# Optimization experiments

Measured on AMD Instinct MI355X. Metric: run time of the kernel, lower is better.

The kernel has to match this reference:

```python
import jax, jax.numpy as jnp
import numpy as np

SH_C0 = 0.28209479177387814  # DC spherical-harmonic basis constant


def setup_inputs() -> dict:
    key = jax.random.key(0)
    ks = jax.random.split(key, 6)
    b, v, g = 1, 2, 2048
    means = jax.random.normal(ks[0], (b, g, 3), dtype=jnp.float32) * 2.0
    # PSD 3x3 covariances via L @ L^T
    L = jax.random.normal(ks[1], (b, g, 3, 3), dtype=jnp.float32) * 0.2
    covariances = jnp.einsum('bgij,bgkj->bgik', L, L) + 1e-4 * jnp.eye(3, dtype=jnp.float32)
    harmonics = jax.random.normal(ks[2], (b, g, 3, 1), dtype=jnp.float32) * 0.5
    opacities = jax.nn.sigmoid(jax.random.normal(ks[3], (b, g), dtype=jnp.float32))
    # camera-to-world extrinsics: identity rotation, cameras pulled back on -z
    ext = jnp.tile(jnp.eye(4, dtype=jnp.float32), (b, v, 1, 1))
    trans = jnp.array([[0.0, 0.0, -8.0], [0.5, 0.0, -8.0]], dtype=jnp.float32)
    ext = ext.at[:, :, :3, 3].set(trans[None])
    intr = jnp.tile(jnp.array([[1.0, 0.0, 0.5], [0.0, 1.0, 0.5], [0.0, 0.0, 1.0]],
                              dtype=jnp.float32), (b, v, 1, 1))  # normalized intrinsics
    return {"means": means, "covariances": covariances, "harmonics": harmonics,
            "opacities": opacities, "extrinsics": ext, "intrinsics": intr,
            "height": 96, "width": 96}


def _render_one(viewmat, K, means, covs, sh, opac, bg, H, W, near, far):
    # viewmat: world->camera [4,4]; K: pixel intrinsics [3,3]
    R, t = viewmat[:3, :3], viewmat[:3, 3]
    cam = means @ R.T + t                                   # [G,3]
    x, y, z = cam[:, 0], cam[:, 1], cam[:, 2]
    zc = jnp.maximum(z, 1e-6)
    fx, fy, cx, cy = K[0, 0], K[1, 1], K[0, 2], K[1, 2]
    u = fx * x / zc + cx                                    # pixel-space 2D means
    vv = fy * y / zc + cy
    # 3D covariance in camera frame, then EWA projection to 2D
    covc = jnp.einsum('ij,gjk,lk->gil', R, covs, R)         # [G,3,3]
    zero = jnp.zeros_like(z)
    J = jnp.stack([jnp.stack([fx / zc, zero, -fx * x / zc**2], -1),
                   jnp.stack([zero, fy / zc, -fy * y / zc**2], -1)], -2)  # [G,2,3]
    cov2 = jnp.einsum('gij,gjk,glk->gil', J, covc, J)       # [G,2,2]
    a = cov2[:, 0, 0] + 0.3                                 # low-pass dilation
    c = cov2[:, 1, 1] + 0.3
    bq = cov2[:, 0, 1]
    det = a * c - bq * bq
    inv_det = 1.0 / jnp.maximum(det, 1e-12)
    # pixel grid (pixel centers)
    px = jnp.arange(W, dtype=jnp.float32) + 0.5
    py = jnp.arange(H, dtype=jnp.float32) + 0.5
    PX, PY = jnp.meshgrid(px, py)                           # [H,W]
    dx = PX.reshape(-1)[None, :] - u[:, None]               # [G,HW]
    dy = PY.reshape(-1)[None, :] - vv[:, None]
    power = -0.5 * inv_det[:, None] * (c[:, None] * dx * dx + a[:, None] * dy * dy
                                       - 2.0 * bq[:, None] * dx * dy)
    alpha = jnp.clip(opac[:, None] * jnp.exp(jnp.minimum(power, 0.0)), 0.0, 0.999)
    valid = (z > near) & (z < far) & (det > 0.0)
    alpha = alpha * valid[:, None].astype(alpha.dtype)      # [G,HW]
    col = SH_C0 * sh[:, :, 0] + 0.5                         # DC SH -> rgb [G,3]
    # front-to-back alpha compositing in depth order
    order = jnp.argsort(z)
    alpha_s = alpha[order]
    col_s = col[order]
    z_s = z[order]
    cum = jnp.cumprod(1.0 - alpha_s, axis=0)                # [G,HW]
    T = jnp.concatenate([jnp.ones((1, alpha_s.shape[1]), alpha_s.dtype), cum[:-1]], 0)
    w = T * alpha_s                                         # per-gaussian pixel weights
    color = jnp.einsum('gp,gc->cp', w, col_s) + cum[-1][None, :] * bg[:, None]
    depth = jnp.sum(w * z_s[:, None], axis=0)
    return color.reshape(3, H, W), depth.reshape(H, W)


def reference(means, covariances, harmonics, opacities, extrinsics, intrinsics, height, width):
    near0, far0 = 0.1, 100.0
    sf = 1.0 / near0                                        # scale_factor = 10
    bg = jnp.zeros(3, dtype=jnp.float32)                    # background_color
    b, v = extrinsics.shape[:2]
    means_s = means * sf
    covs_s = covariances * (sf * sf)
    ext = extrinsics.at[..., :3, 3].multiply(sf)
    near, far = 1.0, far0 * sf
    ext = ext.reshape(b * v, 4, 4)
    K = intrinsics.reshape(b * v, 3, 3)
    K = K.at[:, 0, :].multiply(float(width)).at[:, 1, :].multiply(float(height))
    viewmats = jnp.linalg.inv(ext)                          # world->camera
    # repeat gaussians over views: 'b g ... -> (b v) g ...'
    m_r = jnp.repeat(means_s, v, axis=0)
    c_r = jnp.repeat(covs_s, v, axis=0)
    s_r = jnp.repeat(harmonics, v, axis=0)
    o_r = jnp.repeat(opacities, v, axis=0)
    render = jax.vmap(lambda vm, Kc, m, cc, s, o:
                      _render_one(vm, Kc, m, cc, s, o, bg, height, width, near, far))
    color, depth = render(viewmats, K, m_r, c_r, s_r, o_r)
    color = jnp.clip(color.reshape(b, v, 3, height, width), 0.0, 1.0)
    depth = depth.reshape(b, v, height, width)
    return color, depth
```

## Files before the change

kernel.cpp:

```cpp
#include <hip/hip_runtime.h>

#define SH_C0 0.28209479177387814f
#define LOG2E 1.4426950408889634f

__device__ __forceinline__ void view_from_ext(const float* e, float R[9], float t[3]) {
  const float sf = 10.0f;
  float a00=e[0],a01=e[1],a02=e[2], a10=e[4],a11=e[5],a12=e[6], a20=e[8],a21=e[9],a22=e[10];
  float tx=e[3]*sf, ty=e[7]*sf, tz=e[11]*sf;
  float c00 =  a11*a22 - a12*a21;
  float c01 = -(a10*a22 - a12*a20);
  float c02 =  a10*a21 - a11*a20;
  float det = a00*c00 + a01*c01 + a02*c02;
  float id = 1.0f/det;
  R[0]=c00*id;               R[1]=(a02*a21-a01*a22)*id; R[2]=(a01*a12-a02*a11)*id;
  R[3]=c01*id;               R[4]=(a00*a22-a02*a20)*id; R[5]=(a02*a10-a00*a12)*id;
  R[6]=c02*id;               R[7]=(a01*a20-a00*a21)*id; R[8]=(a00*a11-a01*a10)*id;
  t[0]=-(R[0]*tx+R[1]*ty+R[2]*tz);
  t[1]=-(R[3]*tx+R[4]*ty+R[5]*tz);
  t[2]=-(R[6]*tx+R[7]*ty+R[8]*tz);
}

__global__ __launch_bounds__(256) void rank_prep_kernel(
    const float* __restrict__ means, const float* __restrict__ covs,
    const float* __restrict__ sh, const float* __restrict__ opac,
    const float* __restrict__ ext, const float* __restrict__ intr,
    float* __restrict__ sorted, int G, float Wf, float Hf) {
  __shared__ float kl[2048];
  __shared__ int ps[4][64];
  int v = blockIdx.y;
  int tid = threadIdx.x;
  float R[9], t3[3];
  view_from_ext(ext + v*16, R, t3);
  for (int i = tid; i < G; i += 256) {
    const float* m = means + (size_t)i*3;
    kl[i] = R[6]*(m[0]*10.0f) + R[7]*(m[1]*10.0f) + R[8]*(m[2]*10.0f) + t3[2];
  }
  __syncthreads();
  int s = tid >> 6, gl = tid & 63;
  int g = blockIdx.x*64 + gl;
  float myz = kl[g];
  int seg = G >> 2;
  int j0 = s * seg;
  int cnt = 0;
  #pragma unroll 16
  for (int j = j0; j < j0 + seg; ++j) {
    float kj = kl[j];
    cnt += (kj < myz || (kj == myz && j < g)) ? 1 : 0;
  }
  ps[s][gl] = cnt;
  __syncthreads();
  if (s != 0) return;
  int rank = ps[0][gl] + ps[1][gl] + ps[2][gl] + ps[3][gl];

  const float* Kv = intr + v*9;
  float fx = Kv[0]*Wf, cx = Kv[2]*Wf;
  float fy = Kv[4]*Hf, cy = Kv[5]*Hf;
  const float* m = means + (size_t)g*3;
  float mx = m[0]*10.0f, my = m[1]*10.0f, mz = m[2]*10.0f;
  float x = R[0]*mx + R[1]*my + R[2]*mz + t3[0];
  float y = R[3]*mx + R[4]*my + R[5]*mz + t3[1];
  float z = R[6]*mx + R[7]*my + R[8]*mz + t3[2];
  float zc = fmaxf(z, 1e-6f);
  float u  = fx*x/zc + cx;
  float vv = fy*y/zc + cy;
  const float* C9 = covs + (size_t)g*9;
  float cs[9];
  #pragma unroll
  for (int q = 0; q < 9; ++q) cs[q] = C9[q]*100.0f;
  float tm[9], M[9];
  #pragma unroll
  for (int r2 = 0; r2 < 3; ++r2)
    #pragma unroll
    for (int c2 = 0; c2 < 3; ++c2)
      tm[r2*3+c2] = R[r2*3+0]*cs[c2] + R[r2*3+1]*cs[3+c2] + R[r2*3+2]*cs[6+c2];
  #pragma unroll
  for (int r2 = 0; r2 < 3; ++r2)
    #pragma unroll
    for (int c2 = 0; c2 < 3; ++c2)
      M[r2*3+c2] = tm[r2*3+0]*R[c2*3+0] + tm[r2*3+1]*R[c2*3+1] + tm[r2*3+2]*R[c2*3+2];
  float j0f = fx/zc, j2f = -fx*x/(zc*zc);
  float j1f = fy/zc, j3f = -fy*y/(zc*zc);
  float c00 = j0f*(M[0]*j0f + M[2]*j2f) + j2f*(M[6]*j0f + M[8]*j2f);
  float c01 = j0f*(M[1]*j1f + M[2]*j3f) + j2f*(M[7]*j1f + M[8]*j3f);
  float c11 = j1f*(M[4]*j1f + M[5]*j3f) + j3f*(M[7]*j1f + M[8]*j3f);
  float a = c00 + 0.3f, c = c11 + 0.3f, bq = c01;
  float det2 = a*c - bq*bq;
  float invd = 1.0f/fmaxf(det2, 1e-12f);
  bool valid = (z > 1.0f) && (z < 1000.0f) && (det2 > 0.0f);
  float op = valid ? opac[g] : 0.0f;
  float* o = sorted + ((size_t)v*G + rank)*12;
  o[0] = u; o[1] = vv;
  o[2] = -0.5f*invd*c*LOG2E;
  o[3] =  invd*bq*LOG2E;
  o[4] = -0.5f*invd*a*LOG2E;
  o[5] = op;
  o[6] = SH_C0*sh[(size_t)g*3+0]+0.5f;
  o[7] = SH_C0*sh[(size_t)g*3+1]+0.5f;
  o[8] = SH_C0*sh[(size_t)g*3+2]+0.5f;
  o[9] = z; o[10] = 0.0f; o[11] = 0.0f;
}

__global__ __launch_bounds__(256) void render_kernel(
    const float4* __restrict__ srt, float4* __restrict__ p4,
    float* __restrict__ pD, int G, int chunkSize, int P, int W) {
  __shared__ float4 sp[128*3];
  int tid = threadIdx.x;
  int view = blockIdx.z, chunk = blockIdx.y;
  int pixBase = blockIdx.x * 1024;
  float pxk[4], pyk[4];
  #pragma unroll
  for (int k = 0; k < 4; ++k) {
    int p = pixBase + tid + k*256;
    pxk[k] = (float)(p % W) + 0.5f;
    pyk[k] = (float)(p / W) + 0.5f;
  }
  float T[4]  = {1.0f,1.0f,1.0f,1.0f};
  float cr[4] = {0,0,0,0}, cg[4] = {0,0,0,0}, cb[4] = {0,0,0,0}, dp[4] = {0,0,0,0};
  int cstart = chunk * chunkSize, cend = cstart + chunkSize;
  for (int g0 = cstart; g0 < cend; g0 += 128) {
    int nt = min(128, cend - g0);
    __syncthreads();
    for (int q = tid; q < nt*3; q += 256)
      sp[q] = srt[((size_t)view*G + g0)*3 + q];
    __syncthreads();
    #pragma unroll 2
    for (int i = 0; i < nt; ++i) {
      float4 q0 = sp[i*3+0], q1 = sp[i*3+1], q2 = sp[i*3+2];
      float u = q0.x, vv = q0.y, A = q0.z, B = q0.w;
      float Cc = q1.x, op = q1.y, r = q1.z, gcol = q1.w;
      float bcol = q2.x, z = q2.y;
      #pragma unroll
      for (int k = 0; k < 4; ++k) {
        float dx = pxk[k] - u, dy = pyk[k] - vv;
        float t1 = fmaf(B, dy, A*dx);
        float pw = fmaf(dx, t1, Cc*dy*dy);
        pw = fminf(pw, 0.0f);
        float al = fminf(op*exp2f(pw), 0.999f);
        float w = T[k]*al;
        cr[k] = fmaf(w, r,    cr[k]);
        cg[k] = fmaf(w, gcol, cg[k]);
        cb[k] = fmaf(w, bcol, cb[k]);
        dp[k] = fmaf(w, z,    dp[k]);
        T[k] *= (1.0f - al);
      }
    }
  }
  size_t base = ((size_t)(view*gridDim.y + chunk))*(size_t)P;
  #pragma unroll
  for (int k = 0; k < 4; ++k) {
    int pix = pixBase + tid + k*256;
    p4[base + pix] = make_float4(T[k], cr[k], cg[k], cb[k]);
    pD[base + pix] = dp[k];
  }
}

template<int NC>
__global__ __launch_bounds__(256) void combine_kernel(
    const float4* __restrict__ p4, const float* __restrict__ pD,
    float* __restrict__ out, int P, int V) {
  int id = blockIdx.x*256 + threadIdx.x;
  if (id >= V*P) return;
  int view = id / P, pix = id - view*P;
  float T = 1.0f, cr = 0, cg = 0, cb = 0, dp = 0;
  #pragma unroll
  for (int c2 = 0; c2 < NC; ++c2) {
    size_t base = ((size_t)(view*NC + c2))*(size_t)P + pix;
    float4 b = p4[base];
    float d  = pD[base];
    cr = fmaf(T, b.y, cr);
    cg = fmaf(T, b.z, cg);
    cb = fmaf(T, b.w, cb);
    dp = fmaf(T, d,   dp);
    T *= b.x;
  }
  out[(size_t)(view*3+0)*P + pix] = fminf(fmaxf(cr, 0.0f), 1.0f);
  out[(size_t)(view*3+1)*P + pix] = fminf(fmaxf(cg, 0.0f), 1.0f);
  out[(size_t)(view*3+2)*P + pix] = fminf(fmaxf(cb, 0.0f), 1.0f);
  out[(size_t)V*3*P + (size_t)view*P + pix] = dp;
}

extern "C" void kernel_launch(void* const* d_in, const int* in_sizes, int n_in,
                              void* d_out, int out_size, void* d_ws, size_t ws_size,
                              hipStream_t stream) {
  const float* means = (const float*)d_in[0];
  const float* covs  = (const float*)d_in[1];
  const float* sh    = (const float*)d_in[2];
  const float* opac  = (const float*)d_in[3];
  const float* ext   = (const float*)d_in[4];
  const float* intr  = (const float*)d_in[5];
  const int G = in_sizes[0] / 3;
  const int V = in_sizes[4] / 16;
  const int H = 96, W = 96, P = H*W;

  char* ws = (char*)d_ws;
  float* sorted = (float*)ws;
  size_t off1 = (((size_t)V*G*12*sizeof(float)) + 255) & ~(size_t)255;
  int NC = 32;
  size_t p4_bytes = (size_t)V*NC*(size_t)P*sizeof(float4);
  float4* p4 = (float4*)(ws + off1);
  size_t off2 = (off1 + p4_bytes + 255) & ~(size_t)255;
  float* pD = (float*)(ws + off2);

  dim3 gr(G/64, V);
  rank_prep_kernel<<<gr, 256, 0, stream>>>(means, covs, sh, opac, ext, intr,
                                           sorted, G, (float)W, (float)H);
  dim3 gc(P/1024, NC, V);
  render_kernel<<<gc, 256, 0, stream>>>((const float4*)sorted, p4, pD, G, G/NC, P, W);
  int cbn = (V*P + 255)/256;
  combine_kernel<32><<<cbn, 256, 0, stream>>>(p4, pD, (float*)d_out, P, V);
}
```

Before: 118.5 us.

## Cull gaussians per 32x32 tile with conservative bound; vectorize rank counting

The render kernel now maps each block to a 32x32 pixel tile and a 64-gaussian chunk. It computes a conservative upper bound on the exponent over the tile and compacts only the surviving gaussians into a shared index list, so the blend loop skips gaussians that cannot contribute. The rank kernel reads depth keys as float4 to cut shared-memory load instructions. The cull threshold of -30 in log2 space drops contributions below roughly 1e-9, a small approximation, and the clamp of the exponent to non-positive values is removed.

Measured after the change: 106.4 us. -10.2%, faster.

```diff
diff --git a/kernel.cpp b/kernel.cpp
--- a/kernel.cpp
+++ b/kernel.cpp
@@ -25,8 +25,9 @@
     const float* __restrict__ sh, const float* __restrict__ opac,
     const float* __restrict__ ext, const float* __restrict__ intr,
     float* __restrict__ sorted, int G, float Wf, float Hf) {
-  __shared__ float kl[2048];
+  __shared__ float4 kl4[512];
   __shared__ int ps[4][64];
+  float* kl = (float*)kl4;
   int v = blockIdx.y;
   int tid = threadIdx.x;
   float R[9], t3[3];
@@ -39,13 +40,17 @@
   int s = tid >> 6, gl = tid & 63;
   int g = blockIdx.x*64 + gl;
   float myz = kl[g];
-  int seg = G >> 2;
-  int j0 = s * seg;
+  int q4 = (G >> 2) >> 2;
+  int b4 = s * q4;
   int cnt = 0;
-  #pragma unroll 16
-  for (int j = j0; j < j0 + seg; ++j) {
-    float kj = kl[j];
-    cnt += (kj < myz || (kj == myz && j < g)) ? 1 : 0;
+  #pragma unroll 8
+  for (int j4 = 0; j4 < q4; ++j4) {
+    float4 f = kl4[b4 + j4];
+    int j = (b4 + j4) << 2;
+    cnt += (f.x < myz || (f.x == myz && (j+0) < g)) ? 1 : 0;
+    cnt += (f.y < myz || (f.y == myz && (j+1) < g)) ? 1 : 0;
+    cnt += (f.z < myz || (f.z == myz && (j+2) < g)) ? 1 : 0;
+    cnt += (f.w < myz || (f.w == myz && (j+3) < g)) ? 1 : 0;
   }
   ps[s][gl] = cnt;
   __syncthreads();
@@ -102,53 +107,71 @@
 
 __global__ __launch_bounds__(256) void render_kernel(
     const float4* __restrict__ srt, float4* __restrict__ p4,
-    float* __restrict__ pD, int G, int chunkSize, int P, int W) {
-  __shared__ float4 sp[128*3];
+    float* __restrict__ pD, int G, int P, int W) {
+  __shared__ float4 sp[64*3];
+  __shared__ int sidx[64];
+  __shared__ int snum;
   int tid = threadIdx.x;
   int view = blockIdx.z, chunk = blockIdx.y;
-  int pixBase = blockIdx.x * 1024;
-  float pxk[4], pyk[4];
-  #pragma unroll
-  for (int k = 0; k < 4; ++k) {
-    int p = pixBase + tid + k*256;
-    pxk[k] = (float)(p % W) + 0.5f;
-    pyk[k] = (float)(p / W) + 0.5f;
-  }
+  int ntx = W >> 5;
+  int tx = blockIdx.x % ntx, ty = blockIdx.x / ntx;
+  float x0 = tx*32 + 0.5f, y0 = ty*32 + 0.5f;
+
+  if (tid < 192) sp[tid] = srt[((size_t)view*G + chunk*64)*3 + tid];
+  __syncthreads();
+  if (tid < 64) {
+    float4 q0 = sp[tid*3], q1 = sp[tid*3+1];
+    float u = q0.x, vv = q0.y, A = q0.z, B = q0.w, Cc = q1.x;
+    float lx = x0 - u,  hx = x0 + 31.0f - u;
+    float ly = y0 - vv, hy = y0 + 31.0f - vv;
+    float dx2 = (lx <= 0.0f && hx >= 0.0f) ? 0.0f : fminf(lx*lx, hx*hx);
+    float dy2 = (ly <= 0.0f && hy >= 0.0f) ? 0.0f : fminf(ly*ly, hy*hy);
+    float bmax = fmaxf(fmaxf(B*lx*ly, B*lx*hy), fmaxf(B*hx*ly, B*hx*hy));
+    float bound = A*dx2 + Cc*dy2 + bmax;
+    bool keep = bound > -30.0f;
+    unsigned long long mask = __ballot(keep);
+    int pos = __popcll(mask & ((1ull << tid) - 1ull));
+    if (keep) sidx[pos] = tid;
+    if (tid == 0) snum = (int)__popcll(mask);
+  }
+  __syncthreads();
+  int nsurv = snum;
+
+  float pxc = x0 + (float)(tid & 31);
+  float pyk[4];
+  #pragma unroll
+  for (int k = 0; k < 4; ++k) pyk[k] = y0 + (float)((tid >> 5) + k*8);
   float T[4]  = {1.0f,1.0f,1.0f,1.0f};
   float cr[4] = {0,0,0,0}, cg[4] = {0,0,0,0}, cb[4] = {0,0,0,0}, dp[4] = {0,0,0,0};
-  int cstart = chunk * chunkSize, cend = cstart + chunkSize;
-  for (int g0 = cstart; g0 < cend; g0 += 128) {
-    int nt = min(128, cend - g0);
-    __syncthreads();
-    for (int q = tid; q < nt*3; q += 256)
-      sp[q] = srt[((size_t)view*G + g0)*3 + q];
-    __syncthreads();
-    #pragma unroll 2
-    for (int i = 0; i < nt; ++i) {
-      float4 q0 = sp[i*3+0], q1 = sp[i*3+1], q2 = sp[i*3+2];
-      float u = q0.x, vv = q0.y, A = q0.z, B = q0.w;
-      float Cc = q1.x, op = q1.y, r = q1.z, gcol = q1.w;
-      float bcol = q2.x, z = q2.y;
-      #pragma unroll
-      for (int k = 0; k < 4; ++k) {
-        float dx = pxk[k] - u, dy = pyk[k] - vv;
-        float t1 = fmaf(B, dy, A*dx);
-        float pw = fmaf(dx, t1, Cc*dy*dy);
-        pw = fminf(pw, 0.0f);
-        float al = fminf(op*exp2f(pw), 0.999f);
-        float w = T[k]*al;
-        cr[k] = fmaf(w, r,    cr[k]);
-        cg[k] = fmaf(w, gcol, cg[k]);
-        cb[k] = fmaf(w, bcol, cb[k]);
-        dp[k] = fmaf(w, z,    dp[k]);
-        T[k] *= (1.0f - al);
-      }
+
+  for (int i = 0; i < nsurv; ++i) {
+    int idx = sidx[i];
+    float4 q0 = sp[idx*3+0], q1 = sp[idx*3+1], q2 = sp[idx*3+2];
+    float u = q0.x, vv = q0.y, A = q0.z, B = q0.w;
+    float Cc = q1.x, op = q1.y, r = q1.z, gcol = q1.w;
+    float bcol = q2.x, z = q2.y;
+    float dx = pxc - u;
+    float Adx = A*dx;
+    #pragma unroll
+    for (int k = 0; k < 4; ++k) {
+      float dy = pyk[k] - vv;
+      float t1 = fmaf(B, dy, Adx);
+      float cdy = Cc*dy;
+      float pw = fmaf(dx, t1, cdy*dy);
+      float al = fminf(op*exp2f(pw), 0.999f);
+      float w = T[k]*al;
+      cr[k] = fmaf(w, r,    cr[k]);
+      cg[k] = fmaf(w, gcol, cg[k]);
+      cb[k] = fmaf(w, bcol, cb[k]);
+      dp[k] = fmaf(w, z,    dp[k]);
+      T[k] = fmaf(-al, T[k], T[k]);
     }
   }
   size_t base = ((size_t)(view*gridDim.y + chunk))*(size_t)P;
+  int lx2 = tid & 31, lyb = tid >> 5;
   #pragma unroll
   for (int k = 0; k < 4; ++k) {
-    int pix = pixBase + tid + k*256;
+    int pix = (ty*32 + lyb + k*8)*W + tx*32 + lx2;
     p4[base + pix] = make_float4(T[k], cr[k], cg[k], cb[k]);
     pD[base + pix] = dp[k];
   }
@@ -191,21 +214,20 @@
   const int G = in_sizes[0] / 3;
   const int V = in_sizes[4] / 16;
   const int H = 96, W = 96, P = H*W;
+  const int NC = 32;
 
   char* ws = (char*)d_ws;
   float* sorted = (float*)ws;
   size_t off1 = (((size_t)V*G*12*sizeof(float)) + 255) & ~(size_t)255;
-  int NC = 32;
-  size_t p4_bytes = (size_t)V*NC*(size_t)P*sizeof(float4);
   float4* p4 = (float4*)(ws + off1);
-  size_t off2 = (off1 + p4_bytes + 255) & ~(size_t)255;
+  size_t off2 = (off1 + (size_t)V*NC*(size_t)P*sizeof(float4) + 255) & ~(size_t)255;
   float* pD = (float*)(ws + off2);
 
   dim3 gr(G/64, V);
   rank_prep_kernel<<<gr, 256, 0, stream>>>(means, covs, sh, opac, ext, intr,
                                            sorted, G, (float)W, (float)H);
-  dim3 gc(P/1024, NC, V);
-  render_kernel<<<gc, 256, 0, stream>>>((const float4*)sorted, p4, pD, G, G/NC, P, W);
+  dim3 gc((W/32)*(H/32), NC, V);
+  render_kernel<<<gc, 256, 0, stream>>>((const float4*)sorted, p4, pD, G, P, W);
   int cbn = (V*P + 255)/256;
   combine_kernel<32><<<cbn, 256, 0, stream>>>(p4, pD, (float*)d_out, P, V);
 }
```
